# Kernel tuning notes

Hardware: AMD Instinct MI355X
Metric: run time of the kernel (lower is better)

The kernel has to match this reference:

```python
import jax, jax.numpy as jnp
import numpy as np

B, N, DIM = 4, 2048, 512
H, DH = 8, 64  # n_heads, dim_head; inner = H*DH = 512
SCALE = DH ** -0.5


def setup_inputs() -> dict:
    key = jax.random.key(0)
    k1, k2, k3 = jax.random.split(key, 3)
    inner = H * DH
    X = jax.random.normal(k1, (B, N, DIM), dtype=jnp.float32)
    W_qkv = jax.random.normal(k2, (DIM, 3 * inner), dtype=jnp.float32) * (DIM ** -0.5)
    W_out = jax.random.normal(k3, (inner, DIM), dtype=jnp.float32) * (inner ** -0.5)
    b_out = jnp.zeros((DIM,), dtype=jnp.float32)
    return {"X": X, "W_qkv": W_qkv, "W_out": W_out, "b_out": b_out}


def reference(X, W_qkv, W_out, b_out):
    # X: (b, n, dim)
    qkv = X @ W_qkv                      # (b, n, 3*h*d)
    q, k, v = jnp.split(qkv, 3, axis=-1)
    def to_heads(t):
        b, n, _ = t.shape
        return t.reshape(b, n, H, DH).transpose(0, 2, 1, 3)  # (b, h, n, d)
    q, k, v = to_heads(q), to_heads(k), to_heads(v)
    # NOTE: original computes scores[n, m] = k_n . q_m and softmaxes over m (query axis)
    scores = jnp.einsum('bhnd,bhmd->bhnm', k, q) * SCALE     # (b, h, n_k, m_q)
    att = jax.nn.softmax(scores, axis=-1)
    # out token axis is the KEY index n: out[n, d] = sum_e att[n, e] * v[e, d]
    out = jnp.einsum('bhne,bhed->bhnd', att, v)              # (b, h, n, d)
    out = out.transpose(0, 2, 1, 3).reshape(X.shape[0], X.shape[1], H * DH)  # (b, n, h*d)
    return out @ W_out + b_out
```

## Files before the change

### kernel.cpp

```cpp
#include <hip/hip_runtime.h>
#include <hip/hip_bf16.h>

typedef __bf16 bf16_t;
typedef bf16_t bf16x8 __attribute__((ext_vector_type(8)));
typedef bf16_t bf16x4v __attribute__((ext_vector_type(4)));
typedef float f32x4 __attribute__((ext_vector_type(4)));
typedef float f32x16 __attribute__((ext_vector_type(16)));
typedef int i32x4 __attribute__((ext_vector_type(4)));

#define B_SZ 4
#define N_TOK 2048
#define DIM 512
#define H_N 8
#define DH 64
#define INNER 512
#define M_ROWS 8192
#define NQKV 1536
#define K_FOLD 0.18033688011112042f

#define GLD_LDS16(gp, lp)                                          \
  __builtin_amdgcn_global_load_lds(                                \
      (const __attribute__((address_space(1))) void*)(gp),         \
      (__attribute__((address_space(3))) void*)(lp), 16, 0, 0)

__device__ __forceinline__ float fexp2(float x) {
#if __has_builtin(__builtin_amdgcn_exp2f)
  return __builtin_amdgcn_exp2f(x);
#else
  float r;
  asm volatile("v_exp_f32 %0, %1\n\ts_nop 1" : "=v"(r) : "v"(x));
  return r;
#endif
}

__device__ __forceinline__ int cvtpk_bf16(float lo, float hi) {
  int r;
  asm("v_cvt_pk_bf16_f32 %0, %1, %2" : "=v"(r) : "v"(lo), "v"(hi));
  return r;
}

__device__ __forceinline__ void permswap32(int& a, int& b) {
  asm volatile("v_permlane32_swap_b32 %0, %1" : "+v"(a), "+v"(b));
}


__global__ void f32_to_bf16_kernel(const float* __restrict__ src,
                                   bf16_t* __restrict__ dst, int n4) {
  int i = blockIdx.x * blockDim.x + threadIdx.x;
  int stride = gridDim.x * blockDim.x;
  for (; i < n4; i += stride) {
    float4 f = reinterpret_cast<const float4*>(src)[i];
    bf16x4v o;
    o.x = (bf16_t)f.x; o.y = (bf16_t)f.y; o.z = (bf16_t)f.z; o.w = (bf16_t)f.w;
    reinterpret_cast<bf16x4v*>(dst)[i] = o;
  }
}

__global__ void transpose_f32_to_bf16_kernel(const float* __restrict__ src,
                                             bf16_t* __restrict__ dst, int R, int C) {
  int t = blockIdx.x * blockDim.x + threadIdx.x;
  if (t >= R * C) return;
  int r = t / C, c = t - r * C;
  dst[(size_t)c * R + r] = (bf16_t)src[t];
}

template <int MODE>
__global__ __launch_bounds__(256) void gemm_bf16_kernel(
    const bf16_t* __restrict__ A, const bf16_t* __restrict__ Bt,
    int M, int Nn, int K,
    bf16_t* __restrict__ qb, bf16_t* __restrict__ kb, bf16_t* __restrict__ vtb,
    float* __restrict__ outF, const float* __restrict__ bias) {
  __shared__ bf16_t As[128 * 64];
  __shared__ bf16_t Bs[128 * 64];

  const int tid = threadIdx.x;
  const int lane = tid & 63;
  const int wave = tid >> 6;
  const int g = lane >> 4, c = lane & 15;
  const int wm = (wave >> 1) * 64, wn = (wave & 1) * 64;
  const int m0 = blockIdx.x * 128, n0 = blockIdx.y * 128;

  f32x4 acc[4][4] = {};

  for (int k0 = 0; k0 < K; k0 += 64) {
    __syncthreads();
    #pragma unroll
    for (int i = 0; i < 4; ++i) {
      int blk = i * 256 + tid;
      int row = blk >> 3;
      int cb = (blk & 7) ^ (row & 7);
      int base = (i * 256 + wave * 64) * 8;
      GLD_LDS16(A + (size_t)(m0 + row) * K + k0 + cb * 8, &As[base]);
      GLD_LDS16(Bt + (size_t)(n0 + row) * K + k0 + cb * 8, &Bs[base]);
    }
    __syncthreads();
    __builtin_amdgcn_s_setprio(1);
    #pragma unroll
    for (int ks = 0; ks < 2; ++ks) {
      bf16x8 af[4], bfr[4];
      #pragma unroll
      for (int i = 0; i < 4; ++i) {
        af[i] = *reinterpret_cast<const bf16x8*>(
            &As[(wm + i * 16 + c) * 64 + (((ks * 4 + g) ^ (c & 7)) * 8)]);
        bfr[i] = *reinterpret_cast<const bf16x8*>(
            &Bs[(wn + i * 16 + c) * 64 + (((ks * 4 + g) ^ (c & 7)) * 8)]);
      }
      #pragma unroll
      for (int mi = 0; mi < 4; ++mi)
        #pragma unroll
        for (int ni = 0; ni < 4; ++ni)
          acc[mi][ni] = __builtin_amdgcn_mfma_f32_16x16x32_bf16(
              af[mi], bfr[ni], acc[mi][ni], 0, 0, 0);
    }
    __builtin_amdgcn_s_setprio(0);
  }

  #pragma unroll
  for (int mi = 0; mi < 4; ++mi) {
    #pragma unroll
    for (int ni = 0; ni < 4; ++ni) {
      int colg = n0 + wn + ni * 16 + c;
      if (MODE == 0) {
        int s = colg >> 9;
        int hh = (colg >> 6) & 7, dd = colg & 63;
        int rowg0 = m0 + wm + mi * 16 + g * 4;
        int bb = rowg0 >> 11, nn = rowg0 & 2047;
        if (s == 2) {
          bf16x4v pk;
          pk.x = (bf16_t)acc[mi][ni][0];
          pk.y = (bf16_t)acc[mi][ni][1];
          pk.z = (bf16_t)acc[mi][ni][2];
          pk.w = (bf16_t)acc[mi][ni][3];
          *reinterpret_cast<bf16x4v*>(
              &vtb[(((size_t)(bb * H_N + hh)) * DH + dd) * N_TOK + nn]) = pk;
        } else {
          float sc = (s == 1) ? K_FOLD : 1.0f;
          bf16_t* dst = (s == 0) ? qb : kb;
          #pragma unroll
          for (int r = 0; r < 4; ++r)
            dst[(((size_t)(bb * H_N + hh)) * N_TOK + nn + r) * DH + dd] =
                (bf16_t)(acc[mi][ni][r] * sc);
        }
      } else {
        #pragma unroll
        for (int r = 0; r < 4; ++r) {
          int rowg = m0 + wm + mi * 16 + g * 4 + r;
          outF[(size_t)rowg * Nn + colg] = acc[mi][ni][r] + bias[colg];
        }
      }
    }
  }
}

__global__ __launch_bounds__(256, 2) void attn_kernel(
    const bf16_t* __restrict__ Qproj, const bf16_t* __restrict__ Kproj,
    const bf16_t* __restrict__ Vt, bf16_t* __restrict__ att_out) {
  const int glin = blockIdx.x;
  const int xcd = glin & 7;
  const int jj = glin >> 3;
  const int hb = xcd * 4 + (jj >> 4);
  const int rb = jj & 15;
  const int h = hb & 7, b = hb >> 3;

  const size_t hbo = (size_t)(b * H_N + h);
  const bf16_t* Aq = Kproj + hbo * N_TOK * DH;
  const bf16_t* Ak = Qproj + hbo * N_TOK * DH;
  const bf16_t* Av = Vt + hbo * (size_t)DH * N_TOK;

  const int tid = threadIdx.x, lane = tid & 63, wave = tid >> 6;
  const int nl = lane & 31;
  const int hf = lane >> 5;
  const int r0 = rb * 128, wr0 = wave * 32;

  __shared__ bf16_t sK[2][128 * 64];
  __shared__ bf16_t sV[2][64 * 128];

  bf16x8 qreg[4];
  #pragma unroll
  for (int ks = 0; ks < 4; ++ks)
    qreg[ks] = *reinterpret_cast<const bf16x8*>(
        &Aq[(size_t)(r0 + wr0 + nl) * DH + ks * 16 + hf * 8]);

  bf16x8 ones;
  #pragma unroll
  for (int i = 0; i < 8; ++i) ones[i] = (bf16_t)1.0f;

  f32x16 accO0 = {}, accO1 = {};
  f32x16 accL = {};

  auto stage = [&](bf16_t* dK, bf16_t* dV, int j0) {
    #pragma unroll
    for (int i = 0; i < 4; ++i) {
      int idx = i * 256 + tid;
      int base = (i * 256 + wave * 64) * 8;
      int rowK = idx >> 3;
      int cbK = (idx & 7) ^ (rowK & 7);
      GLD_LDS16(Ak + (size_t)(j0 + rowK) * DH + cbK * 8, dK + base);
      int rowV = idx >> 4;
      int sv = idx & 15;
      int pV = (sv & 8) | ((sv & 7) ^ (rowV & 7));
      GLD_LDS16(Av + (size_t)rowV * N_TOK + j0 + pV * 8, dV + base);
    }
  };

  stage(sK[0], sV[0], 0);
  __syncthreads();

  constexpr int NT = N_TOK / 128;
  for (int t = 0; t < NT; ++t) {
    if (t + 1 < NT) stage(sK[(t + 1) & 1], sV[(t + 1) & 1], (t + 1) * 128);
    const bf16_t* bK = sK[t & 1];
    const bf16_t* bV = sV[t & 1];

    f32x16 aT[2][2] = {};
    __builtin_amdgcn_s_setprio(1);
    #pragma unroll
    for (int ch = 0; ch < 2; ++ch) {
      #pragma unroll
      for (int ks = 0; ks < 4; ++ks) {
        #pragma unroll
        for (int mi = 0; mi < 2; ++mi) {
          int rowt = ch * 64 + mi * 32 + nl;
          bf16x8 ak = *reinterpret_cast<const bf16x8*>(
              &bK[rowt * 64 + (((ks * 2 + hf) ^ (rowt & 7)) * 8)]);
          aT[ch][mi] = __builtin_amdgcn_mfma_f32_32x32x16_bf16(
              ak, qreg[ks], aT[ch][mi], 0, 0, 0);
        }
      }
    }
    __builtin_amdgcn_s_setprio(0);

    #pragma unroll
    for (int ch = 0; ch < 2; ++ch)
      #pragma unroll
      for (int mi = 0; mi < 2; ++mi)
        #pragma unroll
        for (int r = 0; r < 16; ++r)
          aT[ch][mi][r] = fexp2(aT[ch][mi][r]);

    i32x4 pk[2][4];
    #pragma unroll
    for (int ch = 0; ch < 2; ++ch) {
      #pragma unroll
      for (int ks = 0; ks < 4; ++ks) {
        const int mi = ks >> 1, base = (ks & 1) * 8;
        int a0 = cvtpk_bf16(aT[ch][mi][base + 0], aT[ch][mi][base + 1]);
        int b0 = cvtpk_bf16(aT[ch][mi][base + 4], aT[ch][mi][base + 5]);
        int a1 = cvtpk_bf16(aT[ch][mi][base + 2], aT[ch][mi][base + 3]);
        int b1 = cvtpk_bf16(aT[ch][mi][base + 6], aT[ch][mi][base + 7]);
        permswap32(a0, b0);
        permswap32(a1, b1);
        pk[ch][ks].x = a0; pk[ch][ks].y = a1; pk[ch][ks].z = b0; pk[ch][ks].w = b1;
      }
    }

    __builtin_amdgcn_s_setprio(1);
    #pragma unroll
    for (int ch = 0; ch < 2; ++ch) {
      #pragma unroll
      for (int ks = 0; ks < 4; ++ks) {
        bf16x8 pfrag = __builtin_bit_cast(bf16x8, pk[ch][ks]);
        int pp = ch * 8 + ks * 2 + hf;
        int rv0 = nl, rv1 = 32 + nl;
        bf16x8 av0 = *reinterpret_cast<const bf16x8*>(
            &bV[rv0 * 128 + (((pp & 8) | ((pp & 7) ^ (rv0 & 7))) * 8)]);
        bf16x8 av1 = *reinterpret_cast<const bf16x8*>(
            &bV[rv1 * 128 + (((pp & 8) | ((pp & 7) ^ (rv1 & 7))) * 8)]);
        accO0 = __builtin_amdgcn_mfma_f32_32x32x16_bf16(av0, pfrag, accO0, 0, 0, 0);
        accO1 = __builtin_amdgcn_mfma_f32_32x32x16_bf16(av1, pfrag, accO1, 0, 0, 0);
        accL  = __builtin_amdgcn_mfma_f32_32x32x16_bf16(ones, pfrag, accL, 0, 0, 0);
      }
    }
    __builtin_amdgcn_s_setprio(0);

    __syncthreads();
  }

  float invL = 1.0f / accL[0];
  const int nrow = r0 + wr0 + nl;
  #pragma unroll
  for (int q = 0; q < 4; ++q) {
    int d0a = 8 * q + 4 * hf;
    bf16x4v o;
    o.x = (bf16_t)(accO0[4 * q + 0] * invL);
    o.y = (bf16_t)(accO0[4 * q + 1] * invL);
    o.z = (bf16_t)(accO0[4 * q + 2] * invL);
    o.w = (bf16_t)(accO0[4 * q + 3] * invL);
    *reinterpret_cast<bf16x4v*>(
        &att_out[((size_t)(b * N_TOK) + nrow) * INNER + h * DH + d0a]) = o;
    bf16x4v o2;
    o2.x = (bf16_t)(accO1[4 * q + 0] * invL);
    o2.y = (bf16_t)(accO1[4 * q + 1] * invL);
    o2.z = (bf16_t)(accO1[4 * q + 2] * invL);
    o2.w = (bf16_t)(accO1[4 * q + 3] * invL);
    *reinterpret_cast<bf16x4v*>(
        &att_out[((size_t)(b * N_TOK) + nrow) * INNER + h * DH + 32 + d0a]) = o2;
  }
}


extern "C" void kernel_launch(void* const* d_in, const int* in_sizes, int n_in,
                              void* d_out, int out_size, void* d_ws, size_t ws_size,
                              hipStream_t stream) {
  const float* X    = (const float*)d_in[0];
  const float* Wqkv = (const float*)d_in[1];
  const float* Wout = (const float*)d_in[2];
  const float* bout = (const float*)d_in[3];
  float* out = (float*)d_out;

  char* ws = (char*)d_ws;
  bf16_t* Xb    = (bf16_t*)(ws);
  bf16_t* WqkvT = (bf16_t*)(ws + 8388608);
  bf16_t* WoutT = (bf16_t*)(ws + 9961472);
  bf16_t* Qb    = (bf16_t*)(ws + 10485760);
  bf16_t* Kb    = (bf16_t*)(ws + 18874368);
  bf16_t* Vtb   = (bf16_t*)(ws + 27262976);
  bf16_t* AttO  = (bf16_t*)(ws + 35651584);

  f32_to_bf16_kernel<<<2048, 256, 0, stream>>>(X, Xb, (M_ROWS * DIM) / 4);
  transpose_f32_to_bf16_kernel<<<(DIM * NQKV + 255) / 256, 256, 0, stream>>>(
      Wqkv, WqkvT, DIM, NQKV);
  transpose_f32_to_bf16_kernel<<<(INNER * DIM + 255) / 256, 256, 0, stream>>>(
      Wout, WoutT, INNER, DIM);

  dim3 g1(M_ROWS / 128, NQKV / 128);
  gemm_bf16_kernel<0><<<g1, 256, 0, stream>>>(Xb, WqkvT, M_ROWS, NQKV, DIM,
                                              Qb, Kb, Vtb, nullptr, nullptr);

  attn_kernel<<<dim3(512), 256, 0, stream>>>(Qb, Kb, Vtb, AttO);

  dim3 g3(M_ROWS / 128, DIM / 128);
  gemm_bf16_kernel<1><<<g3, 256, 0, stream>>>(AttO, WoutT, M_ROWS, DIM, DIM,
                                              nullptr, nullptr, nullptr, out, bout);
}
```

Baseline: 93.08 us.

## Store V in MFMA fragment order and load it directly from global

The QKV projection epilogue now writes V in a pre-swizzled layout that matches the MFMA A-operand fragment order for each 128-token tile. The attention kernel then reads V fragments straight from global memory into registers with coalesced 16-byte loads, dropping the V shared-memory staging buffer and its LDS reads. This halves the LDS footprint and removes the V LDS traffic. In exchange, every wave issues its own global loads for the same V tile, with no cross-wave reuse through LDS. Those loads also add latency and register pressure inside the loop, because they are not prefetched a tile ahead.

```diff
diff --git a/kernel.cpp b/kernel.cpp
--- a/kernel.cpp
+++ b/kernel.cpp
@@ -131,8 +131,13 @@
           pk.y = (bf16_t)acc[mi][ni][1];
           pk.z = (bf16_t)acc[mi][ni][2];
           pk.w = (bf16_t)acc[mi][ni][3];
+          int tt = nn >> 7;
+          int chv = (nn >> 6) & 1, ksv = (nn >> 4) & 3, hfv = (nn >> 3) & 1;
+          int vi = dd >> 5, nlv = dd & 31;
           *reinterpret_cast<bf16x4v*>(
-              &vtb[(((size_t)(bb * H_N + hh)) * DH + dd) * N_TOK + nn]) = pk;
+              &vtb[(size_t)(bb * H_N + hh) * (DH * N_TOK)
+                   + tt * 8192 + (vi * 8 + chv * 4 + ksv) * 512
+                   + (hfv * 32 + nlv) * 8 + (nn & 7)]) = pk;
         } else {
           float sc = (s == 1) ? K_FOLD : 1.0f;
           bf16_t* dst = (s == 0) ? qb : kb;
@@ -165,7 +170,7 @@
   const size_t hbo = (size_t)(b * H_N + h);
   const bf16_t* Aq = Kproj + hbo * N_TOK * DH;
   const bf16_t* Ak = Qproj + hbo * N_TOK * DH;
-  const bf16_t* Av = Vt + hbo * (size_t)DH * N_TOK;
+  const bf16_t* Av = Vt + hbo * (size_t)(DH * N_TOK);
 
   const int tid = threadIdx.x, lane = tid & 63, wave = tid >> 6;
   const int nl = lane & 31;
@@ -173,7 +178,6 @@
   const int r0 = rb * 128, wr0 = wave * 32;
 
   __shared__ bf16_t sK[2][128 * 64];
-  __shared__ bf16_t sV[2][64 * 128];
 
   bf16x8 qreg[4];
   #pragma unroll
@@ -188,7 +192,7 @@
   f32x16 accO0 = {}, accO1 = {};
   f32x16 accL = {};
 
-  auto stage = [&](bf16_t* dK, bf16_t* dV, int j0) {
+  auto stageK = [&](bf16_t* dK, int j0) {
     #pragma unroll
     for (int i = 0; i < 4; ++i) {
       int idx = i * 256 + tid;
@@ -196,21 +200,26 @@
       int rowK = idx >> 3;
       int cbK = (idx & 7) ^ (rowK & 7);
       GLD_LDS16(Ak + (size_t)(j0 + rowK) * DH + cbK * 8, dK + base);
-      int rowV = idx >> 4;
-      int sv = idx & 15;
-      int pV = (sv & 8) | ((sv & 7) ^ (rowV & 7));
-      GLD_LDS16(Av + (size_t)rowV * N_TOK + j0 + pV * 8, dV + base);
     }
   };
 
-  stage(sK[0], sV[0], 0);
+  stageK(sK[0], 0);
   __syncthreads();
 
   constexpr int NT = N_TOK / 128;
   for (int t = 0; t < NT; ++t) {
-    if (t + 1 < NT) stage(sK[(t + 1) & 1], sV[(t + 1) & 1], (t + 1) * 128);
+    if (t + 1 < NT) stageK(sK[(t + 1) & 1], (t + 1) * 128);
     const bf16_t* bK = sK[t & 1];
-    const bf16_t* bV = sV[t & 1];
+
+    bf16x8 av[2][2][4];
+    #pragma unroll
+    for (int vi = 0; vi < 2; ++vi)
+      #pragma unroll
+      for (int ch = 0; ch < 2; ++ch)
+        #pragma unroll
+        for (int ks = 0; ks < 4; ++ks)
+          av[vi][ch][ks] = *reinterpret_cast<const bf16x8*>(
+              &Av[(size_t)t * 8192 + (vi * 8 + ch * 4 + ks) * 512 + lane * 8]);
 
     f32x16 aT[2][2] = {};
     __builtin_amdgcn_s_setprio(1);
@@ -260,14 +269,8 @@
       #pragma unroll
       for (int ks = 0; ks < 4; ++ks) {
         bf16x8 pfrag = __builtin_bit_cast(bf16x8, pk[ch][ks]);
-        int pp = ch * 8 + ks * 2 + hf;
-        int rv0 = nl, rv1 = 32 + nl;
-        bf16x8 av0 = *reinterpret_cast<const bf16x8*>(
-            &bV[rv0 * 128 + (((pp & 8) | ((pp & 7) ^ (rv0 & 7))) * 8)]);
-        bf16x8 av1 = *reinterpret_cast<const bf16x8*>(
-            &bV[rv1 * 128 + (((pp & 8) | ((pp & 7) ^ (rv1 & 7))) * 8)]);
-        accO0 = __builtin_amdgcn_mfma_f32_32x32x16_bf16(av0, pfrag, accO0, 0, 0, 0);
-        accO1 = __builtin_amdgcn_mfma_f32_32x32x16_bf16(av1, pfrag, accO1, 0, 0, 0);
+        accO0 = __builtin_amdgcn_mfma_f32_32x32x16_bf16(av[0][ch][ks], pfrag, accO0, 0, 0, 0);
+        accO1 = __builtin_amdgcn_mfma_f32_32x32x16_bf16(av[1][ch][ks], pfrag, accO1, 0, 0, 0);
         accL  = __builtin_amdgcn_mfma_f32_32x32x16_bf16(ones, pfrag, accL, 0, 0, 0);
       }
     }
```

New measurement: 96.04 us. 1.03x slower.

## Split attention KV range across two wave groups and merge partial outputs

Applied to the files above, without the earlier changes.

The attention block grows to 512 threads as two groups of four waves. Each group handles half of the key/value sequence with its own double-buffered LDS tiles of 64 tokens, and the partial outputs and row sums are combined through shared memory at the end. The softmax denominator is now summed with scalar adds of the exponentials, replacing the extra ones-vector MFMA. This doubles in-flight waves per block, which should help hide latency, at the cost of a final LDS reduction, extra barriers and more register pressure under the 512-thread launch bound.

```diff
diff --git a/kernel.cpp b/kernel.cpp
--- a/kernel.cpp
+++ b/kernel.cpp
@@ -152,7 +152,7 @@
   }
 }
 
-__global__ __launch_bounds__(256, 2) void attn_kernel(
+__global__ __launch_bounds__(512, 4) void attn_kernel(
     const bf16_t* __restrict__ Qproj, const bf16_t* __restrict__ Kproj,
     const bf16_t* __restrict__ Vt, bf16_t* __restrict__ att_out) {
   const int glin = blockIdx.x;
@@ -165,15 +165,19 @@
   const size_t hbo = (size_t)(b * H_N + h);
   const bf16_t* Aq = Kproj + hbo * N_TOK * DH;
   const bf16_t* Ak = Qproj + hbo * N_TOK * DH;
-  const bf16_t* Av = Vt + hbo * (size_t)DH * N_TOK;
+  const bf16_t* Av = Vt + hbo * (size_t)(DH * N_TOK);
 
   const int tid = threadIdx.x, lane = tid & 63, wave = tid >> 6;
   const int nl = lane & 31;
   const int hf = lane >> 5;
-  const int r0 = rb * 128, wr0 = wave * 32;
-
-  __shared__ bf16_t sK[2][128 * 64];
-  __shared__ bf16_t sV[2][64 * 128];
+  const int grp = wave >> 2;
+  const int gw = wave & 3;
+  const int r0 = rb * 128, wr0 = gw * 32;
+  const int kv0 = grp * 1024;
+
+  __shared__ __align__(16) char smem[65536];
+  bf16_t* sKg = (bf16_t*)(smem + grp * 32768);
+  bf16_t* sVg = (bf16_t*)(smem + grp * 32768 + 16384);
 
   bf16x8 qreg[4];
   #pragma unroll
@@ -181,120 +185,123 @@
     qreg[ks] = *reinterpret_cast<const bf16x8*>(
         &Aq[(size_t)(r0 + wr0 + nl) * DH + ks * 16 + hf * 8]);
 
-  bf16x8 ones;
-  #pragma unroll
-  for (int i = 0; i < 8; ++i) ones[i] = (bf16_t)1.0f;
-
   f32x16 accO0 = {}, accO1 = {};
-  f32x16 accL = {};
-
-  auto stage = [&](bf16_t* dK, bf16_t* dV, int j0) {
-    #pragma unroll
-    for (int i = 0; i < 4; ++i) {
-      int idx = i * 256 + tid;
-      int base = (i * 256 + wave * 64) * 8;
-      int rowK = idx >> 3;
-      int cbK = (idx & 7) ^ (rowK & 7);
-      GLD_LDS16(Ak + (size_t)(j0 + rowK) * DH + cbK * 8, dK + base);
-      int rowV = idx >> 4;
-      int sv = idx & 15;
-      int pV = (sv & 8) | ((sv & 7) ^ (rowV & 7));
-      GLD_LDS16(Av + (size_t)rowV * N_TOK + j0 + pV * 8, dV + base);
+  float Lp[4] = {};
+
+  const int gtid = tid & 255;
+  auto stage = [&](int buf, int j0) {
+    #pragma unroll
+    for (int i = 0; i < 2; ++i) {
+      int idx = i * 256 + gtid;
+      int row = idx >> 3;
+      int cb = (idx & 7) ^ (row & 7);
+      int base = buf * 4096 + (i * 256 + gw * 64) * 8;
+      GLD_LDS16(Ak + (size_t)(j0 + row) * DH + cb * 8, sKg + base);
+      GLD_LDS16(Av + (size_t)row * N_TOK + j0 + cb * 8, sVg + base);
     }
   };
 
-  stage(sK[0], sV[0], 0);
+  stage(0, kv0);
   __syncthreads();
 
-  constexpr int NT = N_TOK / 128;
+  constexpr int NT = 16;
   for (int t = 0; t < NT; ++t) {
-    if (t + 1 < NT) stage(sK[(t + 1) & 1], sV[(t + 1) & 1], (t + 1) * 128);
-    const bf16_t* bK = sK[t & 1];
-    const bf16_t* bV = sV[t & 1];
-
-    f32x16 aT[2][2] = {};
+    if (t + 1 < NT) stage((t + 1) & 1, kv0 + (t + 1) * 64);
+    const bf16_t* bK = sKg + (t & 1) * 4096;
+    const bf16_t* bV = sVg + (t & 1) * 4096;
+
+    f32x16 aT[2] = {};
     __builtin_amdgcn_s_setprio(1);
     #pragma unroll
-    for (int ch = 0; ch < 2; ++ch) {
+    for (int ks = 0; ks < 4; ++ks) {
       #pragma unroll
-      for (int ks = 0; ks < 4; ++ks) {
-        #pragma unroll
-        for (int mi = 0; mi < 2; ++mi) {
-          int rowt = ch * 64 + mi * 32 + nl;
-          bf16x8 ak = *reinterpret_cast<const bf16x8*>(
-              &bK[rowt * 64 + (((ks * 2 + hf) ^ (rowt & 7)) * 8)]);
-          aT[ch][mi] = __builtin_amdgcn_mfma_f32_32x32x16_bf16(
-              ak, qreg[ks], aT[ch][mi], 0, 0, 0);
-        }
+      for (int mi = 0; mi < 2; ++mi) {
+        int rowt = mi * 32 + nl;
+        bf16x8 ak = *reinterpret_cast<const bf16x8*>(
+            &bK[rowt * 64 + (((ks * 2 + hf) ^ (rowt & 7)) * 8)]);
+        aT[mi] = __builtin_amdgcn_mfma_f32_32x32x16_bf16(
+            ak, qreg[ks], aT[mi], 0, 0, 0);
       }
     }
     __builtin_amdgcn_s_setprio(0);
 
     #pragma unroll
-    for (int ch = 0; ch < 2; ++ch)
-      #pragma unroll
-      for (int mi = 0; mi < 2; ++mi)
-        #pragma unroll
-        for (int r = 0; r < 16; ++r)
-          aT[ch][mi][r] = fexp2(aT[ch][mi][r]);
-
-    i32x4 pk[2][4];
-    #pragma unroll
-    for (int ch = 0; ch < 2; ++ch) {
-      #pragma unroll
-      for (int ks = 0; ks < 4; ++ks) {
-        const int mi = ks >> 1, base = (ks & 1) * 8;
-        int a0 = cvtpk_bf16(aT[ch][mi][base + 0], aT[ch][mi][base + 1]);
-        int b0 = cvtpk_bf16(aT[ch][mi][base + 4], aT[ch][mi][base + 5]);
-        int a1 = cvtpk_bf16(aT[ch][mi][base + 2], aT[ch][mi][base + 3]);
-        int b1 = cvtpk_bf16(aT[ch][mi][base + 6], aT[ch][mi][base + 7]);
-        permswap32(a0, b0);
-        permswap32(a1, b1);
-        pk[ch][ks].x = a0; pk[ch][ks].y = a1; pk[ch][ks].z = b0; pk[ch][ks].w = b1;
-      }
+    for (int r = 0; r < 16; ++r) {
+      float p0 = fexp2(aT[0][r]); aT[0][r] = p0;
+      float p1 = fexp2(aT[1][r]); aT[1][r] = p1;
+      Lp[r & 3] += p0 + p1;
+    }
+
+    i32x4 pk[4];
+    #pragma unroll
+    for (int ks = 0; ks < 4; ++ks) {
+      const int mi = ks >> 1, base = (ks & 1) * 8;
+      int a0 = cvtpk_bf16(aT[mi][base + 0], aT[mi][base + 1]);
+      int b0 = cvtpk_bf16(aT[mi][base + 4], aT[mi][base + 5]);
+      int a1 = cvtpk_bf16(aT[mi][base + 2], aT[mi][base + 3]);
+      int b1 = cvtpk_bf16(aT[mi][base + 6], aT[mi][base + 7]);
+      permswap32(a0, b0);
+      permswap32(a1, b1);
+      pk[ks].x = a0; pk[ks].y = a1; pk[ks].z = b0; pk[ks].w = b1;
     }
 
     __builtin_amdgcn_s_setprio(1);
     #pragma unroll
-    for (int ch = 0; ch < 2; ++ch) {
-      #pragma unroll
-      for (int ks = 0; ks < 4; ++ks) {
-        bf16x8 pfrag = __builtin_bit_cast(bf16x8, pk[ch][ks]);
-        int pp = ch * 8 + ks * 2 + hf;
-        int rv0 = nl, rv1 = 32 + nl;
-        bf16x8 av0 = *reinterpret_cast<const bf16x8*>(
-            &bV[rv0 * 128 + (((pp & 8) | ((pp & 7) ^ (rv0 & 7))) * 8)]);
-        bf16x8 av1 = *reinterpret_cast<const bf16x8*>(
-            &bV[rv1 * 128 + (((pp & 8) | ((pp & 7) ^ (rv1 & 7))) * 8)]);
-        accO0 = __builtin_amdgcn_mfma_f32_32x32x16_bf16(av0, pfrag, accO0, 0, 0, 0);
-        accO1 = __builtin_amdgcn_mfma_f32_32x32x16_bf16(av1, pfrag, accO1, 0, 0, 0);
-        accL  = __builtin_amdgcn_mfma_f32_32x32x16_bf16(ones, pfrag, accL, 0, 0, 0);
-      }
+    for (int ks = 0; ks < 4; ++ks) {
+      bf16x8 pfrag = __builtin_bit_cast(bf16x8, pk[ks]);
+      int rv0 = nl, rv1 = 32 + nl;
+      bf16x8 av0 = *reinterpret_cast<const bf16x8*>(
+          &bV[rv0 * 64 + (((ks * 2 + hf) ^ (rv0 & 7)) * 8)]);
+      bf16x8 av1 = *reinterpret_cast<const bf16x8*>(
+          &bV[rv1 * 64 + (((ks * 2 + hf) ^ (rv1 & 7)) * 8)]);
+      accO0 = __builtin_amdgcn_mfma_f32_32x32x16_bf16(av0, pfrag, accO0, 0, 0, 0);
+      accO1 = __builtin_amdgcn_mfma_f32_32x32x16_bf16(av1, pfrag, accO1, 0, 0, 0);
     }
     __builtin_amdgcn_s_setprio(0);
 
     __syncthreads();
   }
 
-  float invL = 1.0f / accL[0];
-  const int nrow = r0 + wr0 + nl;
-  #pragma unroll
-  for (int q = 0; q < 4; ++q) {
-    int d0a = 8 * q + 4 * hf;
-    bf16x4v o;
-    o.x = (bf16_t)(accO0[4 * q + 0] * invL);
-    o.y = (bf16_t)(accO0[4 * q + 1] * invL);
-    o.z = (bf16_t)(accO0[4 * q + 2] * invL);
-    o.w = (bf16_t)(accO0[4 * q + 3] * invL);
-    *reinterpret_cast<bf16x4v*>(
-        &att_out[((size_t)(b * N_TOK) + nrow) * INNER + h * DH + d0a]) = o;
-    bf16x4v o2;
-    o2.x = (bf16_t)(accO1[4 * q + 0] * invL);
-    o2.y = (bf16_t)(accO1[4 * q + 1] * invL);
-    o2.z = (bf16_t)(accO1[4 * q + 2] * invL);
-    o2.w = (bf16_t)(accO1[4 * q + 3] * invL);
-    *reinterpret_cast<bf16x4v*>(
-        &att_out[((size_t)(b * N_TOK) + nrow) * INNER + h * DH + 32 + d0a]) = o2;
+  float Lsum = (Lp[0] + Lp[1]) + (Lp[2] + Lp[3]);
+  float* mb = (float*)smem;
+  const int moff = (gw * 64 + lane) * 36;
+  if (grp == 1) {
+    #pragma unroll
+    for (int r = 0; r < 16; ++r) {
+      mb[moff + r] = accO0[r];
+      mb[moff + 16 + r] = accO1[r];
+    }
+    mb[moff + 32] = Lsum;
+  }
+  __syncthreads();
+  if (grp == 0) {
+    #pragma unroll
+    for (int r = 0; r < 16; ++r) {
+      accO0[r] += mb[moff + r];
+      accO1[r] += mb[moff + 16 + r];
+    }
+    float l = Lsum + mb[moff + 32];
+    l += __shfl_xor(l, 32);
+    float invL = 1.0f / l;
+    const int nrow = r0 + wr0 + nl;
+    #pragma unroll
+    for (int q = 0; q < 4; ++q) {
+      int d0a = 8 * q + 4 * hf;
+      bf16x4v o;
+      o.x = (bf16_t)(accO0[4 * q + 0] * invL);
+      o.y = (bf16_t)(accO0[4 * q + 1] * invL);
+      o.z = (bf16_t)(accO0[4 * q + 2] * invL);
+      o.w = (bf16_t)(accO0[4 * q + 3] * invL);
+      *reinterpret_cast<bf16x4v*>(
+          &att_out[((size_t)(b * N_TOK) + nrow) * INNER + h * DH + d0a]) = o;
+      bf16x4v o2;
+      o2.x = (bf16_t)(accO1[4 * q + 0] * invL);
+      o2.y = (bf16_t)(accO1[4 * q + 1] * invL);
+      o2.z = (bf16_t)(accO1[4 * q + 2] * invL);
+      o2.w = (bf16_t)(accO1[4 * q + 3] * invL);
+      *reinterpret_cast<bf16x4v*>(
+          &att_out[((size_t)(b * N_TOK) + nrow) * INNER + h * DH + 32 + d0a]) = o2;
+    }
   }
 }
 
@@ -327,7 +334,7 @@
   gemm_bf16_kernel<0><<<g1, 256, 0, stream>>>(Xb, WqkvT, M_ROWS, NQKV, DIM,
                                               Qb, Kb, Vtb, nullptr, nullptr);
 
-  attn_kernel<<<dim3(512), 256, 0, stream>>>(Qb, Kb, Vtb, AttO);
+  attn_kernel<<<dim3(512), 512, 0, stream>>>(Qb, Kb, Vtb, AttO);
 
   dim3 g3(M_ROWS / 128, DIM / 128);
   gemm_bf16_kernel<1><<<g3, 256, 0, stream>>>(AttO, WoutT, M_ROWS, DIM, DIM,
```

Measured after the change: 90.46 us. 1.03x faster.
